# Kernel tuning notes

Hardware: AMD Instinct MI355X
Metric: run time of the kernel (lower is better)

The kernel has to match this reference:

```python
import jax, jax.numpy as jnp
import numpy as np

B, T, D, H = 2048, 200, 128, 128


def setup_inputs() -> dict:
    key = jax.random.key(0)
    k1, k2, k3, k4, k5, k6 = jax.random.split(key, 6)
    inputs = jax.random.normal(k1, (B, T, D), dtype=jnp.float32)
    att_scores = jax.random.uniform(k2, (B, T), dtype=jnp.float32)
    seq_len = jax.random.randint(k3, (B,), 0, T, dtype=jnp.int32)
    s = 1.0 / np.sqrt(D + H)
    Wg = jax.random.normal(k4, (D + H, 2 * H), dtype=jnp.float32) * s
    bg = jnp.ones((2 * H,), dtype=jnp.float32)  # TF GRU gate bias init = 1.0
    Wc = jax.random.normal(k5, (D + H, H), dtype=jnp.float32) * s
    bc = jnp.zeros((H,), dtype=jnp.float32)
    return {"inputs": inputs, "att_scores": att_scores, "seq_len": seq_len,
            "Wg": Wg, "bg": bg, "Wc": Wc, "bc": bc}


def _augru_scan(inputs, att_scores, seq_len, Wg, bg, Wc, bc):
    # time-major xs for scan
    xs = (jnp.swapaxes(inputs, 0, 1),          # [T, B, D]
          jnp.swapaxes(att_scores, 0, 1),      # [T, B]
          jnp.arange(T, dtype=jnp.int32))      # [T]
    h0 = jnp.zeros((inputs.shape[0], H), dtype=inputs.dtype)

    def step(h, x):
        x_t, a_t, t = x
        # gates: sigmoid([x, h] @ Wg + bg) -> reset r, update u
        gi = jax.nn.sigmoid(jnp.concatenate([x_t, h], axis=-1) @ Wg + bg)
        r, u = jnp.split(gi, 2, axis=-1)
        # candidate: tanh([x, r*h] @ Wc + bc)
        c = jnp.tanh(jnp.concatenate([x_t, r * h], axis=-1) @ Wc + bc)
        # attention-gated update (AUGRU): scale update gate by att score
        u = a_t[:, None] * u
        new_h = (1.0 - u) * h + u * c
        # sequence-length masking (TF _rnn_step copy_cond: time >= seq_len)
        valid = (t < seq_len)[:, None]
        out = jnp.where(valid, new_h, jnp.zeros_like(new_h))  # zero_output
        h = jnp.where(valid, new_h, h)                         # carry old state
        return h, out

    final_h, outs = jax.lax.scan(step, h0, xs)
    return jnp.swapaxes(outs, 0, 1)  # [B, T, H]


def reference(inputs, att_scores, seq_len, Wg, bg, Wc, bc):
    return _augru_scan(inputs, att_scores, seq_len, Wg, bg, Wc, bc)
```

## Files before the change

kernel.cpp:

```cpp
#include <hip/hip_runtime.h>
#include <hip/hip_bf16.h>


#define BB   2048
#define TT   200
#define DD   128
#define HH   128
#define NG   256
#define BM   8
#define KP   264
#define RHP  136
#define HP   132
#define UP   132
#define NTH  512

typedef __attribute__((ext_vector_type(8))) __bf16 bf16x8;
typedef __attribute__((ext_vector_type(4))) float  f32x4;

__device__ __forceinline__ unsigned short f2bf(float f) {
    union { float f; unsigned int i; } x; x.f = f;
    unsigned int r = (x.i + 0x7fffu + ((x.i >> 16) & 1u)) >> 16;
    return (unsigned short)r;
}
__device__ __forceinline__ __bf16 f2bfv(float f) {
    union { unsigned short u; __bf16 b; } c; c.u = f2bf(f); return c.b;
}

__global__ __launch_bounds__(NTH, 2)
void augru_kernel(const float* __restrict__ X,
                  const float* __restrict__ ATT,
                  const int*   __restrict__ SL,
                  const float* __restrict__ WG,
                  const float* __restrict__ BG,
                  const float* __restrict__ WC,
                  const float* __restrict__ BC,
                  float*       __restrict__ OUT)
{
    __shared__ unsigned short xs[16 * KP];
    __shared__ unsigned short rh[16 * RHP];
    __shared__ float hs[BM * HP];
    __shared__ float ubuf[BM * UP];
    __shared__ float attall[BM * TT];
    __shared__ float biasg[NG];
    __shared__ float biasc[HH];
    __shared__ int   slbuf[BM];

    const int tid  = threadIdx.x;
    const int wave = tid >> 6;
    const int lane = tid & 63;
    const int quad = lane >> 4;
    const int l16  = lane & 15;
    const int b0   = blockIdx.x * BM;

    for (int i = tid; i < 16 * KP;  i += NTH) xs[i] = 0;
    for (int i = tid; i < 16 * RHP; i += NTH) rh[i] = 0;
    for (int i = tid; i < BM * HP;  i += NTH) hs[i] = 0.f;
    if (tid < NG)                 biasg[tid] = BG[tid];
    else if (tid < NG + HH)       biasc[tid - NG] = BC[tid - NG];
    else if (tid < NG + HH + BM)  slbuf[tid - NG - HH] = SL[b0 + tid - NG - HH];
    for (int tt2 = lane; tt2 < TT; tt2 += 64)
        attall[wave * TT + tt2] = ATT[(long)(b0 + wave) * TT + tt2];

    bf16x8 bgf[2][8];
    bf16x8 bcf[8];
    {
        const int ncol0 = (2 * wave) * 16 + l16;
        const int ncol1 = ncol0 + 16;
        const int nc    = wave * 16 + l16;
        #pragma unroll
        for (int kk = 0; kk < 8; ++kk) {
            bf16x8 t0, t1, t2;
            #pragma unroll
            for (int j = 0; j < 8; ++j) {
                const int k = kk * 32 + quad * 8 + j;
                t0[j] = f2bfv(WG[k * NG + ncol0]);
                t1[j] = f2bfv(WG[k * NG + ncol1]);
                t2[j] = f2bfv(WC[k * HH + nc]);
            }
            bgf[0][kk] = t0; bgf[1][kk] = t1; bcf[kk] = t2;
        }
    }
    __syncthreads();

    int tmax = 0;
    #pragma unroll
    for (int r = 0; r < BM; ++r) tmax = max(tmax, slbuf[r]);

    const int srow = tid >> 5;
    const int sseg = tid & 31;

    float4 xpre;
    if (tid < 256 && tmax > 0)
        xpre = *(const float4*)&X[((long)(b0 + srow) * TT + 0) * DD + sseg * 4];

    for (int t = 0; t < tmax; ++t) {
        if (tid < 256) {
            ushort4 v;
            v.x = f2bf(xpre.x); v.y = f2bf(xpre.y);
            v.z = f2bf(xpre.z); v.w = f2bf(xpre.w);
            *(ushort4*)&xs[srow * KP + sseg * 4] = v;
        }
        __syncthreads();
        if (tid < 256 && t + 1 < tmax)
            xpre = *(const float4*)&X[((long)(b0 + srow) * TT + (t + 1)) * DD + sseg * 4];

        f32x4 accg0 = {0.f,0.f,0.f,0.f}, accg1 = {0.f,0.f,0.f,0.f};
        #pragma unroll
        for (int kk = 0; kk < 8; ++kk) {
            const bf16x8 af = *(const bf16x8*)&xs[l16 * KP + kk * 32 + quad * 8];
            accg0 = __builtin_amdgcn_mfma_f32_16x16x32_bf16(af, bgf[0][kk], accg0, 0, 0, 0);
            accg1 = __builtin_amdgcn_mfma_f32_16x16x32_bf16(af, bgf[1][kk], accg1, 0, 0, 0);
        }
        if (quad < 2) {
            #pragma unroll
            for (int nt2 = 0; nt2 < 2; ++nt2) {
                const f32x4 acc = nt2 ? accg1 : accg0;
                const int colg = (2 * wave + nt2) * 16 + l16;
                #pragma unroll
                for (int reg = 0; reg < 4; ++reg) {
                    const int row = quad * 4 + reg;
                    const float pre = acc[reg] + biasg[colg];
                    const float s = __builtin_amdgcn_rcpf(1.0f + __expf(-pre));
                    if (colg < HH) {
                        rh[row * RHP + colg] = f2bf(s * hs[row * HP + colg]);
                    } else {
                        ubuf[row * UP + (colg - HH)] = attall[row * TT + t] * s;
                    }
                }
            }
        }
        __syncthreads();

        f32x4 accc = {0.f,0.f,0.f,0.f};
        #pragma unroll
        for (int kk = 0; kk < 4; ++kk) {
            const bf16x8 af = *(const bf16x8*)&xs[l16 * KP + kk * 32 + quad * 8];
            accc = __builtin_amdgcn_mfma_f32_16x16x32_bf16(af, bcf[kk], accc, 0, 0, 0);
        }
        #pragma unroll
        for (int kk = 0; kk < 4; ++kk) {
            const bf16x8 af = *(const bf16x8*)&rh[l16 * RHP + kk * 32 + quad * 8];
            accc = __builtin_amdgcn_mfma_f32_16x16x32_bf16(af, bcf[kk + 4], accc, 0, 0, 0);
        }
        if (quad < 2) {
            const int col = wave * 16 + l16;
            #pragma unroll
            for (int reg = 0; reg < 4; ++reg) {
                const int row = quad * 4 + reg;
                float xc = accc[reg] + biasc[col];
                xc = fminf(fmaxf(xc, -15.f), 15.f);
                const float e  = __expf(2.0f * xc);
                const float c  = (e - 1.0f) * __builtin_amdgcn_rcpf(e + 1.0f);
                const float u  = ubuf[row * UP + col];
                const float ho = hs[row * HP + col];
                const float nh = fmaf(u, c - ho, ho);
                const bool valid = t < slbuf[row];
                OUT[((long)(b0 + row) * TT + t) * HH + col] = valid ? nh : 0.f;
                if (valid) {
                    hs[row * HP + col] = nh;
                    xs[row * KP + 128 + col] = f2bf(nh);
                }
            }
        }
        __syncthreads();
    }

    const int n4 = (TT - tmax) * (HH / 4);
    for (int r = 0; r < BM; ++r) {
        float4* p = (float4*)(OUT + ((long)(b0 + r) * TT + tmax) * HH);
        for (int i = tid; i < n4; i += NTH) p[i] = make_float4(0.f, 0.f, 0.f, 0.f);
    }
}

extern "C" void kernel_launch(void* const* d_in, const int* in_sizes, int n_in,
                              void* d_out, int out_size, void* d_ws, size_t ws_size,
                              hipStream_t stream) {
    (void)in_sizes; (void)n_in; (void)d_ws; (void)ws_size; (void)out_size;
    const float* X   = (const float*)d_in[0];
    const float* ATT = (const float*)d_in[1];
    const int*   SL  = (const int*)d_in[2];
    const float* WG  = (const float*)d_in[3];
    const float* BG  = (const float*)d_in[4];
    const float* WC  = (const float*)d_in[5];
    const float* BC  = (const float*)d_in[6];
    float*       OUT = (float*)d_out;
    hipLaunchKernelGGL(augru_kernel, dim3(BB / BM), dim3(NTH), 0, stream,
                       X, ATT, SL, WG, BG, WC, BC, OUT);
}
```

Baseline: 613.4 us.

## Double-buffer x tiles, split MFMA accumulators, and spread gate epilogue across all lanes

Double-buffers the bf16 input tile in shared memory so the next timestep's x is converted and stored during the current step. That removes one barrier per step. The MFMA chains are split into two independent accumulators each to shorten the dependency latency, and the separate h buffer replaces the concatenated layout. The gate and candidate epilogues now use all four quads by shuffling accumulator rows, instead of idling half the lanes. Biases and sequence lengths now live in registers, tanh is written as 1-2/(e+1), and hidden-state stores become unconditional.

```diff
diff --git a/kernel.cpp b/kernel.cpp
--- a/kernel.cpp
+++ b/kernel.cpp
@@ -8,23 +8,18 @@
 #define HH   128
 #define NG   256
 #define BM   8
-#define KP   264
-#define RHP  136
-#define HP   132
-#define UP   132
+#define SB   136
+#define SF   132
 #define NTH  512
 
 typedef __attribute__((ext_vector_type(8))) __bf16 bf16x8;
 typedef __attribute__((ext_vector_type(4))) float  f32x4;
 
-__device__ __forceinline__ unsigned short f2bf(float f) {
-    union { float f; unsigned int i; } x; x.f = f;
-    unsigned int r = (x.i + 0x7fffu + ((x.i >> 16) & 1u)) >> 16;
-    return (unsigned short)r;
-}
-__device__ __forceinline__ __bf16 f2bfv(float f) {
-    union { unsigned short u; __bf16 b; } c; c.u = f2bf(f); return c.b;
-}
+#define MFMA(a, b, c) __builtin_amdgcn_mfma_f32_16x16x32_bf16((a), (b), (c), 0, 0, 0)
+
+union bfu { __bf16 b; unsigned short u; };
+__device__ __forceinline__ unsigned short f2bf(float f) { bfu c; c.b = (__bf16)f; return c.u; }
+__device__ __forceinline__ __bf16 f2bfv(float f) { return (__bf16)f; }
 
 __global__ __launch_bounds__(NTH, 2)
 void augru_kernel(const float* __restrict__ X,
@@ -36,13 +31,12 @@
                   const float* __restrict__ BC,
                   float*       __restrict__ OUT)
 {
-    __shared__ unsigned short xs[16 * KP];
-    __shared__ unsigned short rh[16 * RHP];
-    __shared__ float hs[BM * HP];
-    __shared__ float ubuf[BM * UP];
+    __shared__ unsigned short xb[2][16 * SB];
+    __shared__ unsigned short hb[16 * SB];
+    __shared__ unsigned short rh[16 * SB];
+    __shared__ float hs[BM * SF];
+    __shared__ float ub[BM * SF];
     __shared__ float attall[BM * TT];
-    __shared__ float biasg[NG];
-    __shared__ float biasc[HH];
     __shared__ int   slbuf[BM];
 
     const int tid  = threadIdx.x;
@@ -51,31 +45,35 @@
     const int quad = lane >> 4;
     const int l16  = lane & 15;
     const int b0   = blockIdx.x * BM;
-
-    for (int i = tid; i < 16 * KP;  i += NTH) xs[i] = 0;
-    for (int i = tid; i < 16 * RHP; i += NTH) rh[i] = 0;
-    for (int i = tid; i < BM * HP;  i += NTH) hs[i] = 0.f;
-    if (tid < NG)                 biasg[tid] = BG[tid];
-    else if (tid < NG + HH)       biasc[tid - NG] = BC[tid - NG];
-    else if (tid < NG + HH + BM)  slbuf[tid - NG - HH] = SL[b0 + tid - NG - HH];
-    for (int tt2 = lane; tt2 < TT; tt2 += 64)
-        attall[wave * TT + tt2] = ATT[(long)(b0 + wave) * TT + tt2];
-
-    bf16x8 bgf[2][8];
-    bf16x8 bcf[8];
+    const int qq   = quad & 1;
+    const int top  = quad >> 1;
+    const int r0   = 4 * qq + 2 * top;
+
+    for (int i = tid; i < 2 * 16 * SB; i += NTH) xb[0][i] = 0;
+    for (int i = tid; i < 16 * SB; i += NTH) hb[i] = 0;
+    for (int i = tid; i < 16 * SB; i += NTH) rh[i] = 0;
+    for (int i = tid; i < BM * SF; i += NTH) { hs[i] = 0.f; ub[i] = 0.f; }
+    for (int i = tid; i < BM * TT; i += NTH) attall[i] = ATT[(long)b0 * TT + i];
+    if (tid < BM) slbuf[tid] = SL[b0 + tid];
+
+    const float bgv0 = BG[(2 * wave) * 16 + l16];
+    const float bgv1 = BG[(2 * wave + 1) * 16 + l16];
+    const float bcv  = BC[wave * 16 + l16];
+
+    bf16x8 bgf[2][8], bcf[8];
     {
-        const int ncol0 = (2 * wave) * 16 + l16;
-        const int ncol1 = ncol0 + 16;
-        const int nc    = wave * 16 + l16;
+        const int nc0 = (2 * wave) * 16 + l16;
+        const int nc1 = nc0 + 16;
+        const int ncc = wave * 16 + l16;
         #pragma unroll
         for (int kk = 0; kk < 8; ++kk) {
             bf16x8 t0, t1, t2;
             #pragma unroll
             for (int j = 0; j < 8; ++j) {
                 const int k = kk * 32 + quad * 8 + j;
-                t0[j] = f2bfv(WG[k * NG + ncol0]);
-                t1[j] = f2bfv(WG[k * NG + ncol1]);
-                t2[j] = f2bfv(WC[k * HH + nc]);
+                t0[j] = f2bfv(WG[k * NG + nc0]);
+                t1[j] = f2bfv(WG[k * NG + nc1]);
+                t2[j] = f2bfv(WC[k * HH + ncc]);
             }
             bgf[0][kk] = t0; bgf[1][kk] = t1; bcf[kk] = t2;
         }
@@ -85,81 +83,101 @@
     int tmax = 0;
     #pragma unroll
     for (int r = 0; r < BM; ++r) tmax = max(tmax, slbuf[r]);
+    const int sl0 = slbuf[r0], sl1 = slbuf[r0 + 1];
 
     const int srow = tid >> 5;
     const int sseg = tid & 31;
 
     float4 xpre;
-    if (tid < 256 && tmax > 0)
+    if (tid < 256 && tmax > 0) {
         xpre = *(const float4*)&X[((long)(b0 + srow) * TT + 0) * DD + sseg * 4];
+        ushort4 v; v.x = f2bf(xpre.x); v.y = f2bf(xpre.y); v.z = f2bf(xpre.z); v.w = f2bf(xpre.w);
+        *(ushort4*)&xb[0][srow * SB + sseg * 4] = v;
+        if (tmax > 1)
+            xpre = *(const float4*)&X[((long)(b0 + srow) * TT + 1) * DD + sseg * 4];
+    }
+    __syncthreads();
 
     for (int t = 0; t < tmax; ++t) {
-        if (tid < 256) {
-            ushort4 v;
-            v.x = f2bf(xpre.x); v.y = f2bf(xpre.y);
-            v.z = f2bf(xpre.z); v.w = f2bf(xpre.w);
-            *(ushort4*)&xs[srow * KP + sseg * 4] = v;
-        }
-        __syncthreads();
-        if (tid < 256 && t + 1 < tmax)
-            xpre = *(const float4*)&X[((long)(b0 + srow) * TT + (t + 1)) * DD + sseg * 4];
-
-        f32x4 accg0 = {0.f,0.f,0.f,0.f}, accg1 = {0.f,0.f,0.f,0.f};
-        #pragma unroll
-        for (int kk = 0; kk < 8; ++kk) {
-            const bf16x8 af = *(const bf16x8*)&xs[l16 * KP + kk * 32 + quad * 8];
-            accg0 = __builtin_amdgcn_mfma_f32_16x16x32_bf16(af, bgf[0][kk], accg0, 0, 0, 0);
-            accg1 = __builtin_amdgcn_mfma_f32_16x16x32_bf16(af, bgf[1][kk], accg1, 0, 0, 0);
-        }
-        if (quad < 2) {
+        const unsigned short* xc = &xb[t & 1][0];
+
+        f32x4 a0 = {0.f,0.f,0.f,0.f}, a1 = {0.f,0.f,0.f,0.f};
+        f32x4 a2 = {0.f,0.f,0.f,0.f}, a3 = {0.f,0.f,0.f,0.f};
+        #pragma unroll
+        for (int kk = 0; kk < 4; kk += 2) {
+            const bf16x8 af0 = *(const bf16x8*)&xc[l16 * SB + kk * 32 + quad * 8];
+            const bf16x8 af1 = *(const bf16x8*)&xc[l16 * SB + (kk + 1) * 32 + quad * 8];
+            a0 = MFMA(af0, bgf[0][kk], a0);     a1 = MFMA(af0, bgf[1][kk], a1);
+            a2 = MFMA(af1, bgf[0][kk + 1], a2); a3 = MFMA(af1, bgf[1][kk + 1], a3);
+        }
+        #pragma unroll
+        for (int kk = 4; kk < 8; kk += 2) {
+            const bf16x8 af0 = *(const bf16x8*)&hb[l16 * SB + (kk - 4) * 32 + quad * 8];
+            const bf16x8 af1 = *(const bf16x8*)&hb[l16 * SB + (kk - 3) * 32 + quad * 8];
+            a0 = MFMA(af0, bgf[0][kk], a0);     a1 = MFMA(af0, bgf[1][kk], a1);
+            a2 = MFMA(af1, bgf[0][kk + 1], a2); a3 = MFMA(af1, bgf[1][kk + 1], a3);
+        }
+
+        if (tid < 256 && t + 1 < tmax) {
+            ushort4 v; v.x = f2bf(xpre.x); v.y = f2bf(xpre.y); v.z = f2bf(xpre.z); v.w = f2bf(xpre.w);
+            *(ushort4*)&xb[(t + 1) & 1][srow * SB + sseg * 4] = v;
+            if (t + 2 < tmax)
+                xpre = *(const float4*)&X[((long)(b0 + srow) * TT + (t + 2)) * DD + sseg * 4];
+        }
+
+        const f32x4 g0 = a0 + a2;
+        const f32x4 g1 = a1 + a3;
+        float s20 = __shfl_xor(g0[2], 32, 64), s30 = __shfl_xor(g0[3], 32, 64);
+        float s21 = __shfl_xor(g1[2], 32, 64), s31 = __shfl_xor(g1[3], 32, 64);
+        #pragma unroll
+        for (int nt = 0; nt < 2; ++nt) {
+            const int colg = (2 * wave + nt) * 16 + l16;
+            const float bg = nt ? bgv1 : bgv0;
+            const float v0 = top ? (nt ? s21 : s20) : (nt ? g1[0] : g0[0]);
+            const float v1 = top ? (nt ? s31 : s30) : (nt ? g1[1] : g0[1]);
             #pragma unroll
-            for (int nt2 = 0; nt2 < 2; ++nt2) {
-                const f32x4 acc = nt2 ? accg1 : accg0;
-                const int colg = (2 * wave + nt2) * 16 + l16;
-                #pragma unroll
-                for (int reg = 0; reg < 4; ++reg) {
-                    const int row = quad * 4 + reg;
-                    const float pre = acc[reg] + biasg[colg];
-                    const float s = __builtin_amdgcn_rcpf(1.0f + __expf(-pre));
-                    if (colg < HH) {
-                        rh[row * RHP + colg] = f2bf(s * hs[row * HP + colg]);
-                    } else {
-                        ubuf[row * UP + (colg - HH)] = attall[row * TT + t] * s;
-                    }
+            for (int rr = 0; rr < 2; ++rr) {
+                const int row = r0 + rr;
+                const float pre = (rr ? v1 : v0) + bg;
+                const float s = __builtin_amdgcn_rcpf(1.0f + __expf(-pre));
+                if (wave < 4) {
+                    rh[row * SB + colg] = f2bf(s * hs[row * SF + colg]);
+                } else {
+                    ub[row * SF + (colg - HH)] = attall[row * TT + t] * s;
                 }
             }
         }
         __syncthreads();
 
-        f32x4 accc = {0.f,0.f,0.f,0.f};
+        f32x4 c0 = {0.f,0.f,0.f,0.f}, c1 = {0.f,0.f,0.f,0.f};
         #pragma unroll
         for (int kk = 0; kk < 4; ++kk) {
-            const bf16x8 af = *(const bf16x8*)&xs[l16 * KP + kk * 32 + quad * 8];
-            accc = __builtin_amdgcn_mfma_f32_16x16x32_bf16(af, bcf[kk], accc, 0, 0, 0);
-        }
-        #pragma unroll
-        for (int kk = 0; kk < 4; ++kk) {
-            const bf16x8 af = *(const bf16x8*)&rh[l16 * RHP + kk * 32 + quad * 8];
-            accc = __builtin_amdgcn_mfma_f32_16x16x32_bf16(af, bcf[kk + 4], accc, 0, 0, 0);
-        }
-        if (quad < 2) {
+            const bf16x8 afx = *(const bf16x8*)&xc[l16 * SB + kk * 32 + quad * 8];
+            const bf16x8 afr = *(const bf16x8*)&rh[l16 * SB + kk * 32 + quad * 8];
+            c0 = MFMA(afx, bcf[kk], c0);
+            c1 = MFMA(afr, bcf[kk + 4], c1);
+        }
+        const f32x4 cc = c0 + c1;
+        float t2 = __shfl_xor(cc[2], 32, 64), t3 = __shfl_xor(cc[3], 32, 64);
+
+        {
             const int col = wave * 16 + l16;
+            const float w0 = top ? t2 : cc[0];
+            const float w1 = top ? t3 : cc[1];
             #pragma unroll
-            for (int reg = 0; reg < 4; ++reg) {
-                const int row = quad * 4 + reg;
-                float xc = accc[reg] + biasc[col];
-                xc = fminf(fmaxf(xc, -15.f), 15.f);
-                const float e  = __expf(2.0f * xc);
-                const float c  = (e - 1.0f) * __builtin_amdgcn_rcpf(e + 1.0f);
-                const float u  = ubuf[row * UP + col];
-                const float ho = hs[row * HP + col];
+            for (int rr = 0; rr < 2; ++rr) {
+                const int row = r0 + rr;
+                const float xv = (rr ? w1 : w0) + bcv;
+                const float e  = __expf(2.0f * xv);
+                const float c  = 1.0f - 2.0f * __builtin_amdgcn_rcpf(e + 1.0f);
+                const float u  = ub[row * SF + col];
+                const float ho = hs[row * SF + col];
                 const float nh = fmaf(u, c - ho, ho);
-                const bool valid = t < slbuf[row];
+                const bool valid = t < (rr ? sl1 : sl0);
+                const float hst = valid ? nh : ho;
+                hs[row * SF + col] = hst;
+                hb[row * SB + col] = f2bf(hst);
                 OUT[((long)(b0 + row) * TT + t) * HH + col] = valid ? nh : 0.f;
-                if (valid) {
-                    hs[row * HP + col] = nh;
-                    xs[row * KP + 128 + col] = f2bf(nh);
-                }
             }
         }
         __syncthreads();
```

Measured after the change: 593.1 us. 1.03x faster.
